# Kernel optimization log

Hardware: AMD Instinct MI355X
Metric: run time of the kernel (lower is better)

The kernel has to match this reference:

```python
import jax, jax.numpy as jnp
import numpy as np

N_U, N_R, D, H, E = 100000, 50000, 128, 64, 1000000


def setup_inputs() -> dict:
    key = jax.random.key(0)
    ks = jax.random.split(key, 12)
    s = 1.0 / np.sqrt(D)
    return {
        "x_user": jax.random.normal(ks[0], (N_U, D), jnp.float32),
        "x_res": jax.random.normal(ks[1], (N_R, D), jnp.float32),
        "edge_ua_src": jax.random.randint(ks[2], (E,), 0, N_U),
        "edge_ua_dst": jax.random.randint(ks[3], (E,), 0, N_R),
        "edge_ru_src": jax.random.randint(ks[4], (E,), 0, N_R),
        "edge_ru_dst": jax.random.randint(ks[5], (E,), 0, N_U),
        "W_l_ua": jax.random.normal(ks[6], (D, H), jnp.float32) * s,
        "b_ua": jax.random.normal(ks[7], (H,), jnp.float32) * s,
        "W_r_ua": jax.random.normal(ks[8], (D, H), jnp.float32) * s,
        "W_l_ru": jax.random.normal(ks[9], (D, H), jnp.float32) * s,
        "b_ru": jax.random.normal(ks[10], (H,), jnp.float32) * s,
        "W_r_ru": jax.random.normal(ks[11], (D, H), jnp.float32) * s,
    }


def _sage(x_src, x_dst, src, dst, n_dst, W_l, b_l, W_r):
    # gather neighbor feats, scatter-mean onto dst nodes (0 for isolated nodes)
    agg = jax.ops.segment_sum(x_src[src], dst, num_segments=n_dst)  # [n_dst, D]
    cnt = jax.ops.segment_sum(jnp.ones((src.shape[0], 1), x_src.dtype), dst,
                              num_segments=n_dst)
    mean = agg / jnp.maximum(cnt, 1.0)
    # SAGEConv: lin_l(mean neighbor) + bias + lin_r(self), no bias on lin_r
    return mean @ W_l + b_l + x_dst @ W_r


def reference(x_user, x_res, edge_ua_src, edge_ua_dst, edge_ru_src, edge_ru_dst,
              W_l_ua, b_ua, W_r_ua, W_l_ru, b_ru, W_r_ru):
    out_res = jax.nn.relu(_sage(x_user, x_res, edge_ua_src, edge_ua_dst, N_R,
                                W_l_ua, b_ua, W_r_ua))
    out_user = jax.nn.relu(_sage(x_res, x_user, edge_ru_src, edge_ru_dst, N_U,
                                 W_l_ru, b_ru, W_r_ru))
    return out_user, out_res
```

## Files before the change

kernel.cpp:

```cpp
#include <hip/hip_runtime.h>

#define N_U 100000
#define N_R 50000
#define DIM 128
#define HID 64
#define NE  1000000

#define BROWS 128
#define NB_R ((N_R + BROWS - 1) / BROWS)
#define NB_U ((N_U + BROWS - 1) / BROWS)
#define NBKT (NB_R + NB_U)
#define N_TOT (N_R + N_U)
#define MAXB 800
#define CHUNK 4096
#define BINGRID ((NE + CHUNK - 1) / CHUNK)
#define NBIN (2 * BINGRID)
#define CAPR 3072
#define CAPU 1536
#define SCAP CAPR
#define GU2 ((N_U + 127) / 128)
#define GR2 ((N_R + 127) / 128)
#define NPROJ (GU2 + GR2)
#define NPREP (NBIN + NPROJ)
#define TRIPLE (3 * NBIN)

typedef unsigned int uint;
typedef __attribute__((ext_vector_type(8))) short      bf16x8;
typedef __attribute__((ext_vector_type(4))) float      f32x4;
typedef __attribute__((ext_vector_type(2))) float      f32x2;
typedef __attribute__((ext_vector_type(8))) unsigned short u16x8;

__device__ inline uint bf16_rne(float f) {
    uint u = __float_as_uint(f);
    u += 0x7FFFu + ((u >> 16) & 1u);
    return u >> 16;
}
__device__ inline float bf_lo(uint v) { return __uint_as_float(v << 16); }
__device__ inline float bf_hi(uint v) { return __uint_as_float(v & 0xFFFF0000u); }

__device__ inline uint cvt_pk_bf16(float lo, float hi) {
    uint r;
    asm("v_cvt_pk_bf16_f32 %0, %1, %2" : "=v"(r) : "v"(lo), "v"(hi));
    return r;
}

__device__ inline void pk_acc(f32x2& acc, uint v) {
    f32x2 val;
    val[0] = __uint_as_float(v << 16);
    val[1] = __uint_as_float(v & 0xFFFF0000u);
    asm("v_pk_add_f32 %0, %1, %2" : "+v"(acc) : "v"(val));
}

__device__ inline int bucket_base(int b) {
    return (b < NB_R) ? b * CAPR : NB_R * CAPR + (b - NB_R) * CAPU;
}

__global__ __launch_bounds__(256) void wcvt_kernel(
    const float* __restrict__ Wlua, const float* __restrict__ Wlru,
    const float* __restrict__ Wrua, const float* __restrict__ Wrru,
    unsigned short* __restrict__ Wbf, int* __restrict__ cur)
{
    if (blockIdx.x < 4) {
        const float* Ws[4] = {Wlua, Wlru, Wrua, Wrru};
        const float* W = Ws[blockIdx.x];
        unsigned short* dst = Wbf + blockIdx.x * 8192;
        for (int i = threadIdx.x; i < 1024; i += 256) {
            int k8 = i >> 6, col = i & 63;
            u16x8 p;
#pragma unroll
            for (int j = 0; j < 8; ++j)
                p[j] = (unsigned short)bf16_rne(W[(k8 * 8 + j) * HID + col]);
            *(u16x8*)&dst[i * 8] = p;
        }
    } else {
        int i = (blockIdx.x - 4) * 256 + threadIdx.x;
        if (i < NBKT) cur[i] = 0;
    }
}

__global__ __launch_bounds__(512, 4) void prep_kernel(
    const int* __restrict__ srcA, const int* __restrict__ dstA,
    const int* __restrict__ srcB, const int* __restrict__ dstB,
    int* __restrict__ cur, int* __restrict__ rec,
    const float* __restrict__ xu, const float* __restrict__ xr,
    const unsigned short* __restrict__ Wbf,
    const float* __restrict__ b_ua, const float* __restrict__ b_ru,
    uint* __restrict__ h_user, uint* __restrict__ h_res,
    float* __restrict__ out)
{
    __shared__ __align__(16) uint lds[13312];

    const int bid = blockIdx.x;
    const int t = threadIdx.x;
    int binid = -1, projid = -1;
    if (bid < TRIPLE) {
        if (bid % 3 == 0) binid = bid / 3;
        else projid = (bid / 3) * 2 + (bid % 3 - 1);
    } else {
        projid = 2 * NBIN + (bid - TRIPLE);
    }

    if (binid >= 0) {
        int* cntL = (int*)lds;
        int* offL = cntL + MAXB;
        int* curL = offL + MAXB;
        int* gbase = curL + MAXB;
        int* srec = gbase + MAXB;
        unsigned short* sbkt = (unsigned short*)(srec + CHUNK);
        int* tmp = (int*)(sbkt + CHUNK);

        const int seg = (binid >= BINGRID) ? 1 : 0;
        const int blk = binid - seg * BINGRID;
        const int* __restrict__ src = seg ? srcB : srcA;
        const int* __restrict__ dst = seg ? dstB : dstA;
        const int nbkt   = seg ? NB_U : NB_R;
        const int bktOff = seg ? NB_R : 0;

        const int e0 = blk * CHUNK;
        const int nhere = min(CHUNK, NE - e0);

        for (int i = t; i < nbkt; i += 512) cntL[i] = 0;
        __syncthreads();

        int myB[8], myR[8];
#pragma unroll
        for (int l = 0; l < 8; ++l) {
            int i = e0 + l * 512 + t;
            if (i < NE) {
                int d = dst[i];
                myB[l] = d >> 7;
                myR[l] = ((d & 127) << 17) | src[i];
                atomicAdd(&cntL[myB[l]], 1);
            } else myB[l] = -1;
        }
        __syncthreads();

        int vals[4], s = 0;
#pragma unroll
        for (int l = 0; l < 4; ++l) {
            int idx = t * 4 + l;
            vals[l] = (idx < nbkt) ? cntL[idx] : 0;
            s += vals[l];
        }
        tmp[t] = s;
        __syncthreads();
        for (int o = 1; o < 512; o <<= 1) {
            int v = (t >= o) ? tmp[t - o] : 0;
            __syncthreads();
            tmp[t] += v;
            __syncthreads();
        }
        int run = tmp[t] - s;
#pragma unroll
        for (int l = 0; l < 4; ++l) {
            int idx = t * 4 + l;
            if (idx < nbkt) { offL[idx] = run; curL[idx] = run; }
            run += vals[l];
        }
        __syncthreads();

        for (int i = t; i < nbkt; i += 512)
            if (cntL[i] > 0)
                gbase[i] = bucket_base(bktOff + i) + atomicAdd(&cur[bktOff + i], cntL[i]);

#pragma unroll
        for (int l = 0; l < 8; ++l) {
            if (myB[l] >= 0) {
                int slot = atomicAdd(&curL[myB[l]], 1);
                srec[slot] = myR[l];
                sbkt[slot] = (unsigned short)myB[l];
            }
        }
        __syncthreads();

        for (int sI = t; sI < nhere; sI += 512) {
            int b = sbkt[sI];
            rec[gbase[b] + (sI - offL[b])] = srec[sI];
        }
        return;
    }

    int blk, nrows;
    const float *x, *bias;
    const unsigned short *w0g, *w1g;
    uint* hb; float* ob;
    if (projid < GU2) {
        blk = projid; x = xu; w0g = Wbf; w1g = Wbf + 3 * 8192; bias = b_ru;
        hb = h_user; ob = out; nrows = N_U;
    } else {
        blk = projid - GU2; x = xr; w0g = Wbf + 1 * 8192; w1g = Wbf + 2 * 8192;
        bias = b_ua; hb = h_res; ob = out + (size_t)N_U * HID; nrows = N_R;
    }

    const int rowbase = blk * 128;

    {
        const uint4* s0 = (const uint4*)w0g;
        const uint4* s1 = (const uint4*)w1g;
        uint4* d0 = (uint4*)lds;
        uint4* d1 = (uint4*)(lds + 4096);
        for (int i = t; i < 1024; i += 512) { d0[i] = s0[i]; d1[i] = s1[i]; }
    }

    const int wv = t >> 6, l = t & 63;
    const int lrow = l & 15, lk = l >> 4;
    const int myrow = rowbase + wv * 16 + lrow;
    const bool valid = myrow < nrows;
    const float4* xp = (const float4*)(x + (size_t)myrow * DIM + lk * 8);

    float4 z = make_float4(0.f, 0.f, 0.f, 0.f);
    float4 x0a = z, x0b = z, x1a = z, x1b = z, x2a = z, x2b = z, x3a = z, x3b = z;
    if (valid) {
        x0a = xp[0];  x0b = xp[1];
        x1a = xp[8];  x1b = xp[9];
        x2a = xp[16]; x2b = xp[17];
        x3a = xp[24]; x3b = xp[25];
    }
    __syncthreads();

    f32x4 acc0[4], acc1[4];
#pragma unroll
    for (int n = 0; n < 4; ++n) { acc0[n] = (f32x4)0.f; acc1[n] = (f32x4)0.f; }

#define KKSTEP(KK, XA, XB)                                                        \
    {                                                                             \
        union { uint4 u; bf16x8 v; } af;                                          \
        af.u.x = cvt_pk_bf16(XA.x, XA.y);                                         \
        af.u.y = cvt_pk_bf16(XA.z, XA.w);                                         \
        af.u.z = cvt_pk_bf16(XB.x, XB.y);                                         \
        af.u.w = cvt_pk_bf16(XB.z, XB.w);                                         \
        const int k8 = KK * 4 + lk;                                               \
        _Pragma("unroll")                                                         \
        for (int n = 0; n < 4; ++n) {                                             \
            const int col = n * 16 + lrow;                                        \
            bf16x8 b0 = *(const bf16x8*)&lds[(k8 * 64 + col) * 4];                \
            bf16x8 b1 = *(const bf16x8*)&lds[4096 + (k8 * 64 + col) * 4];         \
            acc0[n] = __builtin_amdgcn_mfma_f32_16x16x32_bf16(af.v, b0, acc0[n], 0, 0, 0); \
            acc1[n] = __builtin_amdgcn_mfma_f32_16x16x32_bf16(af.v, b1, acc1[n], 0, 0, 0); \
        }                                                                         \
    }
    KKSTEP(0, x0a, x0b)
    KKSTEP(1, x1a, x1b)
    KKSTEP(2, x2a, x2b)
    KKSTEP(3, x3a, x3b)
#undef KKSTEP

#pragma unroll
    for (int n = 0; n < 4; ++n) {
        float bv = bias[n * 16 + lrow];
#pragma unroll
        for (int r = 0; r < 4; ++r) acc1[n][r] += bv;
    }

    __syncthreads();
    float* sfp = (float*)lds;
    uint*  hup = lds + 8704;
#pragma unroll
    for (int n = 0; n < 4; ++n) {
#pragma unroll
        for (int r = 0; r < 4; ++r) {
            int row = wv * 16 + lk * 4 + r;
            sfp[row * 68 + n * 16 + lrow] = acc1[n][r];
            float hm = acc0[n][r], ho = __shfl_xor(hm, 1);
            if (!(lrow & 1))
                hup[row * 36 + n * 8 + (lrow >> 1)] = cvt_pk_bf16(hm, ho);
        }
    }
    __syncthreads();
    for (int i = t; i < 128 * 16; i += 512) {
        int r = i >> 4, c = i & 15;
        if (rowbase + r < nrows)
            *(float4*)(ob + (size_t)(rowbase + r) * HID + c * 4) =
                *(const float4*)&sfp[r * 68 + c * 4];
    }
    for (int i = t; i < 128 * 8; i += 512) {
        int r = i >> 3, q = i & 7;
        if (rowbase + r < nrows)
            *(uint4*)(hb + (size_t)(rowbase + r) * 32 + q * 4) =
                *(const uint4*)&hup[r * 36 + q * 4];
    }
}

__global__ __launch_bounds__(256) void csr_all_kernel(
    int* __restrict__ rec, const int* __restrict__ cur, int2* __restrict__ offdeg)
{
    __shared__ int cntL[BROWS], offL[BROWS], curL[BROWS];
    __shared__ int srec[SCAP];
    const int t = threadIdx.x;
    const int bkt = blockIdx.x;
    int degBase, lrow0, nrows, cap;
    if (bkt < NB_R) { degBase = 0;   lrow0 = bkt * BROWS;          nrows = N_R; cap = CAPR; }
    else            { degBase = N_R; lrow0 = (bkt - NB_R) * BROWS; nrows = N_U; cap = CAPU; }

    const int rbase = bucket_base(bkt);
    const int rcnt  = min(cur[bkt], cap);

    if (t < BROWS) cntL[t] = 0;
    __syncthreads();
    for (int i = t; i < rcnt; i += 256) {
        int r = rec[rbase + i];
        srec[i] = r;
        atomicAdd(&cntL[r >> 17], 1);
    }
    __syncthreads();
    if (t < BROWS) offL[t] = cntL[t];
    __syncthreads();
    for (int o = 1; o < BROWS; o <<= 1) {
        int v = (t < BROWS && t >= o) ? offL[t - o] : 0;
        __syncthreads();
        if (t < BROWS) offL[t] += v;
        __syncthreads();
    }
    if (t < BROWS) {
        int excl = offL[t] - cntL[t];
        curL[t] = excl;
        int grow = lrow0 + t;
        if (grow < nrows)
            offdeg[degBase + grow] = make_int2(rbase + excl, cntL[t]);
    }
    __syncthreads();
    for (int i = t; i < rcnt; i += 256) {
        int r = srec[i];
        int slot = atomicAdd(&curL[r >> 17], 1);
        rec[rbase + slot] = r;
    }
}

__global__ __launch_bounds__(256) void gather_all_kernel(
    const uint* __restrict__ hu, const uint* __restrict__ hr,
    const int* __restrict__ rec, const int2* __restrict__ offdeg,
    float* __restrict__ out)
{
    const int sub = threadIdx.x >> 5;
    const int l32 = threadIdx.x & 31;
    const int grow = blockIdx.x * 8 + sub;
    if (grow >= N_TOT) return;

    const uint* __restrict__ h;
    float* orow;
    if (grow < N_R) {
        h = hu;
        orow = out + (size_t)(N_U + grow) * HID;
    } else {
        h = hr;
        orow = out + (size_t)(grow - N_R) * HID;
    }

    const int2 od = offdeg[grow];
    const int o = od.x, d = od.y;
    const int q  = l32 >> 3;
    const int cl = l32 & 7;

    float4 sfA, sfB;
    if (l32 < 8) {
        sfA = *(const float4*)(orow + cl * 8);
        sfB = *(const float4*)(orow + cl * 8 + 4);
    }

    f32x2 A0 = {0.f, 0.f}, A1 = {0.f, 0.f}, A2 = {0.f, 0.f}, A3 = {0.f, 0.f};
#define ACC(v) { pk_acc(A0, v.x); pk_acc(A1, v.y); pk_acc(A2, v.z); pk_acc(A3, v.w); }

    const uint4 z4 = make_uint4(0u, 0u, 0u, 0u);
    for (int j = 0; j < d; j += 32) {
        uint4 v0 = z4, v1 = z4, v2 = z4, v3 = z4;
        uint4 v4 = z4, v5 = z4, v6 = z4, v7 = z4;
        if (j + q < d)      v0 = *(const uint4*)(h + (size_t)(rec[o + j + q] & 0x1FFFF) * 32 + cl * 4);
        if (j + 4 + q < d)  v1 = *(const uint4*)(h + (size_t)(rec[o + j + 4 + q] & 0x1FFFF) * 32 + cl * 4);
        if (j + 8 + q < d)  v2 = *(const uint4*)(h + (size_t)(rec[o + j + 8 + q] & 0x1FFFF) * 32 + cl * 4);
        if (j + 12 + q < d) v3 = *(const uint4*)(h + (size_t)(rec[o + j + 12 + q] & 0x1FFFF) * 32 + cl * 4);
        if (j + 16 + q < d) v4 = *(const uint4*)(h + (size_t)(rec[o + j + 16 + q] & 0x1FFFF) * 32 + cl * 4);
        if (j + 20 + q < d) v5 = *(const uint4*)(h + (size_t)(rec[o + j + 20 + q] & 0x1FFFF) * 32 + cl * 4);
        if (j + 24 + q < d) v6 = *(const uint4*)(h + (size_t)(rec[o + j + 24 + q] & 0x1FFFF) * 32 + cl * 4);
        if (j + 28 + q < d) v7 = *(const uint4*)(h + (size_t)(rec[o + j + 28 + q] & 0x1FFFF) * 32 + cl * 4);
        ACC(v0) ACC(v1) ACC(v2) ACC(v3) ACC(v4) ACC(v5) ACC(v6) ACC(v7)
    }
#undef ACC

#pragma unroll
    for (int off = 8; off <= 16; off <<= 1) {
        A0[0] += __shfl_xor(A0[0], off); A0[1] += __shfl_xor(A0[1], off);
        A1[0] += __shfl_xor(A1[0], off); A1[1] += __shfl_xor(A1[1], off);
        A2[0] += __shfl_xor(A2[0], off); A2[1] += __shfl_xor(A2[1], off);
        A3[0] += __shfl_xor(A3[0], off); A3[1] += __shfl_xor(A3[1], off);
    }

    if (l32 < 8) {
        float invd = 1.0f / fmaxf((float)d, 1.0f);
        float4 rA, rB;
        rA.x = fmaxf(A0[0] * invd + sfA.x, 0.f);
        rA.y = fmaxf(A0[1] * invd + sfA.y, 0.f);
        rA.z = fmaxf(A1[0] * invd + sfA.z, 0.f);
        rA.w = fmaxf(A1[1] * invd + sfA.w, 0.f);
        rB.x = fmaxf(A2[0] * invd + sfB.x, 0.f);
        rB.y = fmaxf(A2[1] * invd + sfB.y, 0.f);
        rB.z = fmaxf(A3[0] * invd + sfB.z, 0.f);
        rB.w = fmaxf(A3[1] * invd + sfB.w, 0.f);
        *(float4*)(orow + cl * 8) = rA;
        *(float4*)(orow + cl * 8 + 4) = rB;
    }
}

extern "C" void kernel_launch(void* const* d_in, const int* in_sizes, int n_in,
                              void* d_out, int out_size, void* d_ws, size_t ws_size,
                              hipStream_t stream)
{
    const float* x_user = (const float*)d_in[0];
    const float* x_res  = (const float*)d_in[1];
    const int* ua_src   = (const int*)d_in[2];
    const int* ua_dst   = (const int*)d_in[3];
    const int* ru_src   = (const int*)d_in[4];
    const int* ru_dst   = (const int*)d_in[5];
    const float* W_l_ua = (const float*)d_in[6];
    const float* b_ua   = (const float*)d_in[7];
    const float* W_r_ua = (const float*)d_in[8];
    const float* W_l_ru = (const float*)d_in[9];
    const float* b_ru   = (const float*)d_in[10];
    const float* W_r_ru = (const float*)d_in[11];

    uint* h_user = (uint*)d_ws;
    uint* h_res  = h_user + (size_t)N_U * 32;
    unsigned short* Wbf = (unsigned short*)(h_res + (size_t)N_R * 32);
    int*  cur    = (int*)(Wbf + 4 * 8192);
    int2* offdeg = (int2*)(cur + NBKT);
    int*  rec    = (int*)(offdeg + N_TOT);

    wcvt_kernel<<<4 + (NBKT + 255) / 256, 256, 0, stream>>>(
        W_l_ua, W_l_ru, W_r_ua, W_r_ru, Wbf, cur);

    prep_kernel<<<NPREP, 512, 0, stream>>>(
        ua_src, ua_dst, ru_src, ru_dst, cur, rec,
        x_user, x_res, Wbf, b_ua, b_ru, h_user, h_res, (float*)d_out);

    csr_all_kernel<<<NBKT, 256, 0, stream>>>(rec, cur, offdeg);

    gather_all_kernel<<<(N_TOT + 7) / 8, 256, 0, stream>>>(
        h_user, h_res, rec, offdeg, (float*)d_out);
}
```

Measured before the change: 100.9 us.

## Fuse CSR build with gather and stage self-term in bf16 scratch

The per-bucket CSR sort and the neighbor gather are merged into one kernel. The sorted edge records now stay in LDS instead of being written back and re-read through a global offset/degree table, which also removes one launch. The self-projection plus bias is stored as bf16 in a workspace buffer rather than as fp32 in the output, halving that write and its later read. The costs are lower precision on the self term, a larger per-block LDS footprint, and reduced gather parallelism because each block processes a whole 128-row bucket with 16 teams.

```diff
diff --git a/kernel.cpp b/kernel.cpp
--- a/kernel.cpp
+++ b/kernel.cpp
@@ -23,6 +23,7 @@
 #define NPROJ (GU2 + GR2)
 #define NPREP (NBIN + NPROJ)
 #define TRIPLE (3 * NBIN)
+#define LDSU 9856
 
 typedef unsigned int uint;
 typedef __attribute__((ext_vector_type(8))) short      bf16x8;
@@ -86,9 +87,9 @@
     const unsigned short* __restrict__ Wbf,
     const float* __restrict__ b_ua, const float* __restrict__ b_ru,
     uint* __restrict__ h_user, uint* __restrict__ h_res,
-    float* __restrict__ out)
+    uint* __restrict__ sbuf)
 {
-    __shared__ __align__(16) uint lds[13312];
+    __shared__ __align__(16) uint lds[LDSU];
 
     const int bid = blockIdx.x;
     const int t = threadIdx.x;
@@ -106,8 +107,8 @@
         int* curL = offL + MAXB;
         int* gbase = curL + MAXB;
         int* srec = gbase + MAXB;
-        unsigned short* sbkt = (unsigned short*)(srec + CHUNK);
-        int* tmp = (int*)(sbkt + CHUNK);
+        unsigned short* sbkt = (unsigned short*)(lds + 7296);
+        int* tmp = (int*)(lds + 9344);
 
         const int seg = (binid >= BINGRID) ? 1 : 0;
         const int blk = binid - seg * BINGRID;
@@ -183,13 +184,13 @@
     int blk, nrows;
     const float *x, *bias;
     const unsigned short *w0g, *w1g;
-    uint* hb; float* ob;
+    uint* hb; uint* sb;
     if (projid < GU2) {
         blk = projid; x = xu; w0g = Wbf; w1g = Wbf + 3 * 8192; bias = b_ru;
-        hb = h_user; ob = out; nrows = N_U;
+        hb = h_user; sb = sbuf; nrows = N_U;
     } else {
         blk = projid - GU2; x = xr; w0g = Wbf + 1 * 8192; w1g = Wbf + 2 * 8192;
-        bias = b_ua; hb = h_res; ob = out + (size_t)N_U * HID; nrows = N_R;
+        bias = b_ua; hb = h_res; sb = sbuf + (size_t)N_U * 32; nrows = N_R;
     }
 
     const int rowbase = blk * 128;
@@ -253,53 +254,62 @@
     }
 
     __syncthreads();
-    float* sfp = (float*)lds;
-    uint*  hup = lds + 8704;
+    uint* hA = lds;
+    uint* hS = lds + 4608;
 #pragma unroll
     for (int n = 0; n < 4; ++n) {
 #pragma unroll
         for (int r = 0; r < 4; ++r) {
             int row = wv * 16 + lk * 4 + r;
-            sfp[row * 68 + n * 16 + lrow] = acc1[n][r];
             float hm = acc0[n][r], ho = __shfl_xor(hm, 1);
-            if (!(lrow & 1))
-                hup[row * 36 + n * 8 + (lrow >> 1)] = cvt_pk_bf16(hm, ho);
-        }
-    }
-    __syncthreads();
-    for (int i = t; i < 128 * 16; i += 512) {
-        int r = i >> 4, c = i & 15;
-        if (rowbase + r < nrows)
-            *(float4*)(ob + (size_t)(rowbase + r) * HID + c * 4) =
-                *(const float4*)&sfp[r * 68 + c * 4];
-    }
+            float sm = acc1[n][r], so = __shfl_xor(sm, 1);
+            if (!(lrow & 1)) {
+                int c2 = n * 8 + (lrow >> 1);
+                hA[row * 36 + c2] = cvt_pk_bf16(hm, ho);
+                hS[row * 36 + c2] = cvt_pk_bf16(sm, so);
+            }
+        }
+    }
+    __syncthreads();
     for (int i = t; i < 128 * 8; i += 512) {
         int r = i >> 3, q = i & 7;
-        if (rowbase + r < nrows)
+        if (rowbase + r < nrows) {
             *(uint4*)(hb + (size_t)(rowbase + r) * 32 + q * 4) =
-                *(const uint4*)&hup[r * 36 + q * 4];
-    }
-}
-
-__global__ __launch_bounds__(256) void csr_all_kernel(
-    int* __restrict__ rec, const int* __restrict__ cur, int2* __restrict__ offdeg)
+                *(const uint4*)&hA[r * 36 + q * 4];
+            *(uint4*)(sb + (size_t)(rowbase + r) * 32 + q * 4) =
+                *(const uint4*)&hS[r * 36 + q * 4];
+        }
+    }
+}
+
+__global__ __launch_bounds__(512) void csr_gather_kernel(
+    const int* __restrict__ rec, const int* __restrict__ cur,
+    const uint* __restrict__ hu, const uint* __restrict__ hr,
+    const uint* __restrict__ sbuf, float* __restrict__ out)
 {
+    __shared__ int srecA[SCAP];
+    __shared__ int srecB[SCAP];
     __shared__ int cntL[BROWS], offL[BROWS], curL[BROWS];
-    __shared__ int srec[SCAP];
+
     const int t = threadIdx.x;
     const int bkt = blockIdx.x;
-    int degBase, lrow0, nrows, cap;
-    if (bkt < NB_R) { degBase = 0;   lrow0 = bkt * BROWS;          nrows = N_R; cap = CAPR; }
-    else            { degBase = N_R; lrow0 = (bkt - NB_R) * BROWS; nrows = N_U; cap = CAPU; }
+    int lrow0, nrows, cap;
+    size_t rowOff;
+    const uint* __restrict__ h;
+    if (bkt < NB_R) {
+        lrow0 = bkt * BROWS; nrows = N_R; cap = CAPR; h = hu; rowOff = N_U;
+    } else {
+        lrow0 = (bkt - NB_R) * BROWS; nrows = N_U; cap = CAPU; h = hr; rowOff = 0;
+    }
 
     const int rbase = bucket_base(bkt);
     const int rcnt  = min(cur[bkt], cap);
 
     if (t < BROWS) cntL[t] = 0;
     __syncthreads();
-    for (int i = t; i < rcnt; i += 256) {
+    for (int i = t; i < rcnt; i += 512) {
         int r = rec[rbase + i];
-        srec[i] = r;
+        srecA[i] = r;
         atomicAdd(&cntL[r >> 17], 1);
     }
     __syncthreads();
@@ -311,92 +321,74 @@
         if (t < BROWS) offL[t] += v;
         __syncthreads();
     }
-    if (t < BROWS) {
-        int excl = offL[t] - cntL[t];
-        curL[t] = excl;
-        int grow = lrow0 + t;
-        if (grow < nrows)
-            offdeg[degBase + grow] = make_int2(rbase + excl, cntL[t]);
-    }
-    __syncthreads();
-    for (int i = t; i < rcnt; i += 256) {
-        int r = srec[i];
+    if (t < BROWS) curL[t] = offL[t] - cntL[t];
+    __syncthreads();
+    for (int i = t; i < rcnt; i += 512) {
+        int r = srecA[i];
         int slot = atomicAdd(&curL[r >> 17], 1);
-        rec[rbase + slot] = r;
-    }
-}
-
-__global__ __launch_bounds__(256) void gather_all_kernel(
-    const uint* __restrict__ hu, const uint* __restrict__ hr,
-    const int* __restrict__ rec, const int2* __restrict__ offdeg,
-    float* __restrict__ out)
-{
-    const int sub = threadIdx.x >> 5;
-    const int l32 = threadIdx.x & 31;
-    const int grow = blockIdx.x * 8 + sub;
-    if (grow >= N_TOT) return;
-
-    const uint* __restrict__ h;
-    float* orow;
-    if (grow < N_R) {
-        h = hu;
-        orow = out + (size_t)(N_U + grow) * HID;
-    } else {
-        h = hr;
-        orow = out + (size_t)(grow - N_R) * HID;
-    }
-
-    const int2 od = offdeg[grow];
-    const int o = od.x, d = od.y;
+        srecB[slot] = r;
+    }
+    __syncthreads();
+
+    const int team = t >> 5, l32 = t & 31;
     const int q  = l32 >> 3;
     const int cl = l32 & 7;
 
-    float4 sfA, sfB;
-    if (l32 < 8) {
-        sfA = *(const float4*)(orow + cl * 8);
-        sfB = *(const float4*)(orow + cl * 8 + 4);
-    }
-
-    f32x2 A0 = {0.f, 0.f}, A1 = {0.f, 0.f}, A2 = {0.f, 0.f}, A3 = {0.f, 0.f};
+    for (int r = team; r < BROWS; r += 16) {
+        const int lr = lrow0 + r;
+        if (lr >= nrows) continue;
+        const int d = cntL[r];
+        const int base = offL[r] - cntL[r];
+        const uint* srow = sbuf + (rowOff + lr) * 32;
+        float* orow = out + (rowOff + lr) * 64;
+
+        float s0 = 0.f, s1 = 0.f, s2 = 0.f, s3 = 0.f;
+        float s4 = 0.f, s5 = 0.f, s6 = 0.f, s7 = 0.f;
+        if (l32 < 8) {
+            uint4 sv = *(const uint4*)(srow + cl * 4);
+            s0 = bf_lo(sv.x); s1 = bf_hi(sv.x); s2 = bf_lo(sv.y); s3 = bf_hi(sv.y);
+            s4 = bf_lo(sv.z); s5 = bf_hi(sv.z); s6 = bf_lo(sv.w); s7 = bf_hi(sv.w);
+        }
+
+        f32x2 A0 = {0.f, 0.f}, A1 = {0.f, 0.f}, A2 = {0.f, 0.f}, A3 = {0.f, 0.f};
 #define ACC(v) { pk_acc(A0, v.x); pk_acc(A1, v.y); pk_acc(A2, v.z); pk_acc(A3, v.w); }
-
-    const uint4 z4 = make_uint4(0u, 0u, 0u, 0u);
-    for (int j = 0; j < d; j += 32) {
-        uint4 v0 = z4, v1 = z4, v2 = z4, v3 = z4;
-        uint4 v4 = z4, v5 = z4, v6 = z4, v7 = z4;
-        if (j + q < d)      v0 = *(const uint4*)(h + (size_t)(rec[o + j + q] & 0x1FFFF) * 32 + cl * 4);
-        if (j + 4 + q < d)  v1 = *(const uint4*)(h + (size_t)(rec[o + j + 4 + q] & 0x1FFFF) * 32 + cl * 4);
-        if (j + 8 + q < d)  v2 = *(const uint4*)(h + (size_t)(rec[o + j + 8 + q] & 0x1FFFF) * 32 + cl * 4);
-        if (j + 12 + q < d) v3 = *(const uint4*)(h + (size_t)(rec[o + j + 12 + q] & 0x1FFFF) * 32 + cl * 4);
-        if (j + 16 + q < d) v4 = *(const uint4*)(h + (size_t)(rec[o + j + 16 + q] & 0x1FFFF) * 32 + cl * 4);
-        if (j + 20 + q < d) v5 = *(const uint4*)(h + (size_t)(rec[o + j + 20 + q] & 0x1FFFF) * 32 + cl * 4);
-        if (j + 24 + q < d) v6 = *(const uint4*)(h + (size_t)(rec[o + j + 24 + q] & 0x1FFFF) * 32 + cl * 4);
-        if (j + 28 + q < d) v7 = *(const uint4*)(h + (size_t)(rec[o + j + 28 + q] & 0x1FFFF) * 32 + cl * 4);
-        ACC(v0) ACC(v1) ACC(v2) ACC(v3) ACC(v4) ACC(v5) ACC(v6) ACC(v7)
-    }
+        const uint4 z4 = make_uint4(0u, 0u, 0u, 0u);
+        for (int j = 0; j < d; j += 16) {
+            uint4 v0 = z4, v1 = z4, v2 = z4, v3 = z4;
+            if (j + q < d)
+                v0 = *(const uint4*)(h + (size_t)(srecB[base + j + q] & 0x1FFFF) * 32 + cl * 4);
+            if (j + 4 + q < d)
+                v1 = *(const uint4*)(h + (size_t)(srecB[base + j + 4 + q] & 0x1FFFF) * 32 + cl * 4);
+            if (j + 8 + q < d)
+                v2 = *(const uint4*)(h + (size_t)(srecB[base + j + 8 + q] & 0x1FFFF) * 32 + cl * 4);
+            if (j + 12 + q < d)
+                v3 = *(const uint4*)(h + (size_t)(srecB[base + j + 12 + q] & 0x1FFFF) * 32 + cl * 4);
+            ACC(v0) ACC(v1) ACC(v2) ACC(v3)
+        }
 #undef ACC
 
 #pragma unroll
-    for (int off = 8; off <= 16; off <<= 1) {
-        A0[0] += __shfl_xor(A0[0], off); A0[1] += __shfl_xor(A0[1], off);
-        A1[0] += __shfl_xor(A1[0], off); A1[1] += __shfl_xor(A1[1], off);
-        A2[0] += __shfl_xor(A2[0], off); A2[1] += __shfl_xor(A2[1], off);
-        A3[0] += __shfl_xor(A3[0], off); A3[1] += __shfl_xor(A3[1], off);
-    }
-
-    if (l32 < 8) {
-        float invd = 1.0f / fmaxf((float)d, 1.0f);
-        float4 rA, rB;
-        rA.x = fmaxf(A0[0] * invd + sfA.x, 0.f);
-        rA.y = fmaxf(A0[1] * invd + sfA.y, 0.f);
-        rA.z = fmaxf(A1[0] * invd + sfA.z, 0.f);
-        rA.w = fmaxf(A1[1] * invd + sfA.w, 0.f);
-        rB.x = fmaxf(A2[0] * invd + sfB.x, 0.f);
-        rB.y = fmaxf(A2[1] * invd + sfB.y, 0.f);
-        rB.z = fmaxf(A3[0] * invd + sfB.z, 0.f);
-        rB.w = fmaxf(A3[1] * invd + sfB.w, 0.f);
-        *(float4*)(orow + cl * 8) = rA;
-        *(float4*)(orow + cl * 8 + 4) = rB;
+        for (int off = 8; off <= 16; off <<= 1) {
+            A0[0] += __shfl_xor(A0[0], off); A0[1] += __shfl_xor(A0[1], off);
+            A1[0] += __shfl_xor(A1[0], off); A1[1] += __shfl_xor(A1[1], off);
+            A2[0] += __shfl_xor(A2[0], off); A2[1] += __shfl_xor(A2[1], off);
+            A3[0] += __shfl_xor(A3[0], off); A3[1] += __shfl_xor(A3[1], off);
+        }
+
+        if (l32 < 8) {
+            float invd = 1.0f / fmaxf((float)d, 1.0f);
+            float4 rA, rB;
+            rA.x = fmaxf(A0[0] * invd + s0, 0.f);
+            rA.y = fmaxf(A0[1] * invd + s1, 0.f);
+            rA.z = fmaxf(A1[0] * invd + s2, 0.f);
+            rA.w = fmaxf(A1[1] * invd + s3, 0.f);
+            rB.x = fmaxf(A2[0] * invd + s4, 0.f);
+            rB.y = fmaxf(A2[1] * invd + s5, 0.f);
+            rB.z = fmaxf(A3[0] * invd + s6, 0.f);
+            rB.w = fmaxf(A3[1] * invd + s7, 0.f);
+            *(float4*)(orow + cl * 8) = rA;
+            *(float4*)(orow + cl * 8 + 4) = rB;
+        }
     }
 }
 
@@ -419,20 +411,18 @@
 
     uint* h_user = (uint*)d_ws;
     uint* h_res  = h_user + (size_t)N_U * 32;
-    unsigned short* Wbf = (unsigned short*)(h_res + (size_t)N_R * 32);
+    uint* sbuf   = h_res + (size_t)N_R * 32;
+    unsigned short* Wbf = (unsigned short*)(sbuf + (size_t)N_TOT * 32);
     int*  cur    = (int*)(Wbf + 4 * 8192);
-    int2* offdeg = (int2*)(cur + NBKT);
-    int*  rec    = (int*)(offdeg + N_TOT);
+    int*  rec    = cur + NBKT;
 
     wcvt_kernel<<<4 + (NBKT + 255) / 256, 256, 0, stream>>>(
         W_l_ua, W_l_ru, W_r_ua, W_r_ru, Wbf, cur);
 
     prep_kernel<<<NPREP, 512, 0, stream>>>(
         ua_src, ua_dst, ru_src, ru_dst, cur, rec,
-        x_user, x_res, Wbf, b_ua, b_ru, h_user, h_res, (float*)d_out);
-
-    csr_all_kernel<<<NBKT, 256, 0, stream>>>(rec, cur, offdeg);
-
-    gather_all_kernel<<<(N_TOT + 7) / 8, 256, 0, stream>>>(
-        h_user, h_res, rec, offdeg, (float*)d_out);
-}
+        x_user, x_res, Wbf, b_ua, b_ru, h_user, h_res, sbuf);
+
+    csr_gather_kernel<<<NBKT, 512, 0, stream>>>(
+        rec, cur, h_user, h_res, sbuf, (float*)d_out);
+}
```

New measurement: 91.12 us. 1.11x faster.
